# Performance work log

Hardware: AMD Instinct MI355X
Metric: run time of the kernel (lower is better)

## Reference

```python
import jax, jax.numpy as jnp
import numpy as np

N = 50000        # nodes
E = 800000       # edges (avg degree 16)
B = 128          # graphs in batch
NODE_F, EDGE_F, GLOB_F = 16, 8, 32
H = 64           # hidden_dim
L = 4            # num_layers
C = 9            # threshold classes
NG, GE = 20, 16  # num gate types, gate embedding dim
MSG_IN = H + EDGE_F + GE   # 88
UPD_IN = 2 * H             # 128


def _ln(x, g, b):
    mu = x.mean(-1, keepdims=True)
    v = ((x - mu) ** 2).mean(-1, keepdims=True)
    return (x - mu) / jnp.sqrt(v + 1e-5) * g + b


def setup_inputs() -> dict:
    key = jax.random.key(0)
    ks = jax.random.split(key, 24)
    w = lambda k, shp: (jax.random.normal(k, shp, jnp.float32) * 0.05)
    inp = {
        'x': jax.random.normal(ks[0], (N, NODE_F), jnp.float32),
        'edge_index': jax.random.randint(ks[1], (2, E), 0, N, jnp.int32),
        'edge_attr': jax.random.normal(ks[2], (E, EDGE_F), jnp.float32),
        'edge_gate_type': jax.random.randint(ks[3], (E,), 0, NG, jnp.int32),
        'batch': jnp.sort(jax.random.randint(ks[4], (N,), 0, B, jnp.int32)),
        'global_features': jax.random.normal(ks[5], (B, GLOB_F), jnp.float32),
        # node_embed
        'W_embed': w(ks[6], (NODE_F, H)), 'b_embed': jnp.zeros((H,), jnp.float32),
        'g_eln': jnp.ones((H,), jnp.float32), 'b_eln': jnp.zeros((H,), jnp.float32),
        # message-passing layers (stacked over L)
        'mp_gate_emb': w(ks[7], (L, NG, GE)),
        'mp_W_msg': w(ks[8], (L, MSG_IN, H)), 'mp_b_msg': jnp.zeros((L, H), jnp.float32),
        'mp_W_upd': w(ks[9], (L, UPD_IN, H)), 'mp_b_upd': jnp.zeros((L, H), jnp.float32),
        # global_proj
        'W_gproj': w(ks[10], (GLOB_F, H)), 'b_gproj': jnp.zeros((H,), jnp.float32),
        'g_gln': jnp.ones((H,), jnp.float32), 'b_gln': jnp.zeros((H,), jnp.float32),
        # combined_mlp
        'W_c1': w(ks[11], (3 * H + H, 2 * H)), 'b_c1': jnp.zeros((2 * H,), jnp.float32),
        'g_cln': jnp.ones((2 * H,), jnp.float32), 'b_cln': jnp.zeros((2 * H,), jnp.float32),
        'W_c2': w(ks[12], (2 * H, H)), 'b_c2': jnp.zeros((H,), jnp.float32),
        # head
        'W_head': w(ks[13], (H, C)), 'b_head': jnp.zeros((C,), jnp.float32),
    }
    return inp


def reference(x, edge_index, edge_attr, edge_gate_type, batch, global_features,
              W_embed, b_embed, g_eln, b_eln,
              mp_gate_emb, mp_W_msg, mp_b_msg, mp_W_upd, mp_b_upd,
              W_gproj, b_gproj, g_gln, b_gln,
              W_c1, b_c1, g_cln, b_cln, W_c2, b_c2, W_head, b_head):
    n_nodes = x.shape[0]
    n_graphs = global_features.shape[0]
    # node embed (dropout = identity in eval)
    h = _ln(jax.nn.relu(x @ W_embed + b_embed), g_eln, b_eln)  # [N,H]
    src, dst = edge_index[0], edge_index[1]
    for l in range(mp_W_msg.shape[0]):
        ge = mp_gate_emb[l][edge_gate_type]                     # [E,GE] gather
        m_in = jnp.concatenate([h[src], edge_attr, ge], axis=-1)  # [E,MSG_IN]
        m = jax.nn.relu(m_in @ mp_W_msg[l] + mp_b_msg[l])          # [E,H]
        agg = jax.ops.segment_sum(m, dst, num_segments=n_nodes)   # [N,H] scatter-add
        h_new = jnp.concatenate([h, agg], axis=-1) @ mp_W_upd[l] + mp_b_upd[l]
        h = h + h_new                                              # residual
    # multi global pooling
    ones = jnp.ones((n_nodes,), h.dtype)
    counts = jax.ops.segment_sum(ones, batch, num_segments=n_graphs)[:, None]
    h_sum = jax.ops.segment_sum(h, batch, num_segments=n_graphs)
    h_mean = h_sum / jnp.maximum(counts, 1.0)
    h_max = jax.ops.segment_max(h, batch, num_segments=n_graphs)
    h_max = jnp.where(counts > 0, h_max, 0.0)
    h_graph = jnp.concatenate([h_mean, h_max, h_sum], axis=-1)   # [B,3H]
    g = _ln(jax.nn.relu(global_features @ W_gproj + b_gproj), g_gln, b_gln)
    c = jnp.concatenate([h_graph, g], axis=-1)                   # [B,4H]
    c = jax.nn.relu(c @ W_c1 + b_c1)
    c = _ln(c, g_cln, b_cln)
    c = jax.nn.relu(c @ W_c2 + b_c2)
    return c @ W_head + b_head                                   # [B,C]
```

## Files before the change

kernel.cpp:

```cpp
#include <hip/hip_runtime.h>

__device__ __forceinline__ int rfl(int v) { return __builtin_amdgcn_readfirstlane(v); }

__device__ __forceinline__ int lower_bound_dev(const int* __restrict__ a, int n, int v) {
  int lo = 0, hi = n;
  while (lo < hi) { int mid = (lo + hi) >> 1; if (a[mid] < v) lo = mid + 1; else hi = mid; }
  return lo;
}

__global__ void zero_kernel(int4* __restrict__ p, int n4) {
  int i = blockIdx.x * 256 + threadIdx.x;
  if (i < n4) p[i] = make_int4(0, 0, 0, 0);
}

__global__ void count_pack_kernel(const int* __restrict__ dst, const int* __restrict__ src,
                                  const int* __restrict__ gt, int* __restrict__ counts,
                                  int* __restrict__ epack0, int E) {
  int e = blockIdx.x * 256 + threadIdx.x;
  if (e < E) {
    atomicAdd(&counts[dst[e]], 1);
    epack0[e] = (gt[e] << 20) | src[e];
  }
}

__global__ __launch_bounds__(256) void scan_phase1(const int* __restrict__ counts,
                                                   int* __restrict__ row_ptr,
                                                   int* __restrict__ blocksums, int n) {
  int tid = threadIdx.x;
  int i0 = blockIdx.x * 1024 + tid * 4;
  int4 c = make_int4(0, 0, 0, 0);
  if (i0 + 3 < n) {
    c = *(const int4*)(counts + i0);
  } else {
    if (i0 + 0 < n) c.x = counts[i0 + 0];
    if (i0 + 1 < n) c.y = counts[i0 + 1];
    if (i0 + 2 < n) c.z = counts[i0 + 2];
    if (i0 + 3 < n) c.w = counts[i0 + 3];
  }
  int s = c.x + c.y + c.z + c.w;
  int lane = tid & 63, wave = tid >> 6;
  int v = s;
  for (int o = 1; o < 64; o <<= 1) { int u = __shfl_up(v, o); if (lane >= o) v += u; }
  __shared__ int wsum[4];
  if (lane == 63) wsum[wave] = v;
  __syncthreads();
  int woff = 0;
  for (int w = 0; w < wave; w++) woff += wsum[w];
  int excl = woff + (v - s);
  if (tid == 255) blocksums[blockIdx.x] = woff + v;
  int p0 = excl, p1 = p0 + c.x, p2 = p1 + c.y, p3 = p2 + c.z;
  if (i0 + 3 < n) {
    *(int4*)(row_ptr + i0) = make_int4(p0, p1, p2, p3);
  } else {
    if (i0 + 0 < n) row_ptr[i0 + 0] = p0;
    if (i0 + 1 < n) row_ptr[i0 + 1] = p1;
    if (i0 + 2 < n) row_ptr[i0 + 2] = p2;
    if (i0 + 3 < n) row_ptr[i0 + 3] = p3;
  }
}

__global__ __launch_bounds__(64) void scan_phase2(int* __restrict__ blocksums, int nb) {
  int carry = 0;
  for (int base = 0; base < nb; base += 64) {
    int i = base + (int)threadIdx.x;
    int v = (i < nb) ? blocksums[i] : 0;
    int inc = v;
    for (int o = 1; o < 64; o <<= 1) { int u = __shfl_up(inc, o); if ((int)threadIdx.x >= o) inc += u; }
    if (i < nb) blocksums[i] = carry + inc - v;
    carry += __shfl(inc, 63);
  }
}

__global__ __launch_bounds__(256) void scan_phase3(int* __restrict__ row_ptr,
                                                   const int* __restrict__ blocksums,
                                                   int* __restrict__ nextp, int n, int E) {
  int i = blockIdx.x * 256 + threadIdx.x;
  if (i < n) {
    int v = row_ptr[i] + blocksums[i >> 10];
    row_ptr[i] = v;
    nextp[i] = v;
  }
  if (i == 0) row_ptr[n] = E;
}

#define SP_EDGES_PER_BLOCK 2048
__global__ __launch_bounds__(256) void scatter_perm_binned(const int* __restrict__ dst,
                                                           int* __restrict__ nextp,
                                                           int* __restrict__ perm,
                                                           int E, int n_nodes) {
  int phase = blockIdx.x & 7;
  int chunk = blockIdx.x >> 3;
  int lo = (int)(((long long)phase * n_nodes) >> 3);
  int hi = (int)(((long long)(phase + 1) * n_nodes) >> 3);
  int base = chunk * SP_EDGES_PER_BLOCK + threadIdx.x * 8;
#pragma unroll
  for (int half = 0; half < 2; half++) {
    int b = base + half * 4;
    if (b >= E) break;
    int4 d;
    if (b + 3 < E) {
      d = *(const int4*)(dst + b);
    } else {
      d.x = dst[b];
      d.y = (b + 1 < E) ? dst[b + 1] : -1;
      d.z = (b + 2 < E) ? dst[b + 2] : -1;
      d.w = (b + 3 < E) ? dst[b + 3] : -1;
    }
    if (d.x >= lo && d.x < hi) { int p = atomicAdd(&nextp[d.x], 1); perm[p] = b + 0; }
    if (d.y >= lo && d.y < hi) { int p = atomicAdd(&nextp[d.y], 1); perm[p] = b + 1; }
    if (d.z >= lo && d.z < hi) { int p = atomicAdd(&nextp[d.z], 1); perm[p] = b + 2; }
    if (d.w >= lo && d.w < hi) { int p = atomicAdd(&nextp[d.w], 1); perm[p] = b + 3; }
  }
}

__global__ void gather_build(const int* __restrict__ perm, const int* __restrict__ epack0,
                             const float* __restrict__ edge_attr,
                             int* __restrict__ epack, float* __restrict__ eap, int E) {
  int idx = blockIdx.x * 256 + threadIdx.x;
  if (idx < E) {
    int e = perm[idx];
    epack[idx] = epack0[e];
    const float4* s = (const float4*)(edge_attr + (size_t)e * 8);
    float4 a0 = s[0], a1 = s[1];
    float4* d = (float4*)(eap + (size_t)idx * 8);
    d[0] = a0; d[1] = a1;
  }
}

__global__ void gew_kernel(const float* __restrict__ gate_emb, const float* __restrict__ W_msg,
                           float* __restrict__ geW, int nrows) {
  int tid = threadIdx.x;
  int lane = tid & 63;
  int row = blockIdx.x * 4 + (tid >> 6);
  if (row >= nrows) return;
  int l = row / 20, t = row % 20;
  const float* ge = gate_emb + ((size_t)l * 20 + t) * 16;
  const float* W3 = W_msg + (size_t)l * 88 * 64 + 72 * 64;
  float acc = 0.f;
#pragma unroll
  for (int k = 0; k < 16; k++) acc = fmaf(ge[k], W3[(size_t)k * 64 + lane], acc);
  geW[(size_t)row * 64 + lane] = acc;
}

__global__ __launch_bounds__(256) void embed_kernel(const float* __restrict__ x,
                                                    const float* __restrict__ W,
                                                    const float* __restrict__ b,
                                                    const float* __restrict__ gamma,
                                                    const float* __restrict__ beta,
                                                    float* __restrict__ h, int n_nodes) {
  __shared__ float Ws[16 * 64];
  int tid = threadIdx.x;
  for (int i = tid; i < 16 * 64; i += 256) Ws[i] = W[i];
  __syncthreads();
  int lane = tid & 63;
  int n = blockIdx.x * 4 + (tid >> 6);
  if (n >= n_nodes) return;
  const float* xr = x + (size_t)n * 16;
  float acc = b[lane];
#pragma unroll
  for (int k = 0; k < 16; k++) acc = fmaf(xr[k], Ws[k * 64 + lane], acc);
  acc = fmaxf(acc, 0.f);
  float s = acc;
  for (int o = 32; o; o >>= 1) s += __shfl_xor(s, o);
  float mu = s * (1.f / 64.f);
  float d = acc - mu;
  float v = d * d;
  for (int o = 32; o; o >>= 1) v += __shfl_xor(v, o);
  float r = rsqrtf(v * (1.f / 64.f) + 1e-5f);
  h[(size_t)n * 64 + lane] = d * r * gamma[lane] + beta[lane];
}

__global__ __launch_bounds__(256) void nodelin_kernel(const float* __restrict__ A,
                                                      const float* __restrict__ W,
                                                      float* __restrict__ C, int n_nodes) {
  __shared__ float As[64 * 64];
  int tid = threadIdx.x;
  int n0 = blockIdx.x * 64;
#pragma unroll
  for (int i = 0; i < 4; i++) {
    int flat = (tid + i * 256) * 4;
    int r = flat >> 6, k = flat & 63;
    float4 f = make_float4(0.f, 0.f, 0.f, 0.f);
    int n = n0 + r;
    if (n < n_nodes) f = *(const float4*)(A + (size_t)n * 64 + k);
    int rp = r ^ (((k >> 2) & 7) << 2);
    As[(k + 0) * 64 + rp] = f.x;
    As[(k + 1) * 64 + rp] = f.y;
    As[(k + 2) * 64 + rp] = f.z;
    As[(k + 3) * 64 + rp] = f.w;
  }
  __syncthreads();
  int tx = tid & 15, ty = tid >> 4;
  float acc[4][4] = {{0.f}};
  const float4* WV = (const float4*)W;
#pragma unroll 4
  for (int k = 0; k < 64; k++) {
    float4 a = *(const float4*)&As[k * 64 + ((ty * 4) ^ (((k >> 2) & 7) << 2))];
    float4 bb = WV[k * 16 + tx];
    float av[4] = {a.x, a.y, a.z, a.w};
    float bv[4] = {bb.x, bb.y, bb.z, bb.w};
#pragma unroll
    for (int i = 0; i < 4; i++)
#pragma unroll
      for (int j = 0; j < 4; j++) acc[i][j] = fmaf(av[i], bv[j], acc[i][j]);
  }
#pragma unroll
  for (int i = 0; i < 4; i++) {
    int n = n0 + ty * 4 + i;
    if (n < n_nodes) {
      float4 o = make_float4(acc[i][0], acc[i][1], acc[i][2], acc[i][3]);
      *(float4*)&C[(size_t)n * 64 + tx * 4] = o;
    }
  }
}

__global__ __launch_bounds__(256, 4) void edge_kernel(const float* __restrict__ hW,
                                                      const int* __restrict__ epack,
                                                      const float* __restrict__ eap,
                                                      const int* __restrict__ row_ptr,
                                                      const float* __restrict__ W_msg_l,
                                                      const float* __restrict__ b_msg_l,
                                                      const float* __restrict__ geW_l,
                                                      float* __restrict__ agg, int n_nodes) {
  int tid = threadIdx.x;
  int lane = tid & 63;
  int n = blockIdx.x * 4 + (tid >> 6);
  if (n >= n_nodes) return;
  float w2[8];
#pragma unroll
  for (int k = 0; k < 8; k++) w2[k] = W_msg_l[(size_t)(64 + k) * 64 + lane];
  float bm = b_msg_l[lane];
  int beg = rfl(row_ptr[n]);
  int end = rfl(row_ptr[n + 1]);
  float acc0 = 0.f, acc1 = 0.f, acc2 = 0.f, acc3 = 0.f;
  int idx = beg;
  for (; idx + 4 <= end; idx += 4) {
    int p0 = rfl(epack[idx + 0]);
    int p1 = rfl(epack[idx + 1]);
    int p2 = rfl(epack[idx + 2]);
    int p3 = rfl(epack[idx + 3]);
    int s0 = p0 & 0xFFFFF, t0 = p0 >> 20;
    int s1 = p1 & 0xFFFFF, t1 = p1 >> 20;
    int s2 = p2 & 0xFFFFF, t2 = p2 >> 20;
    int s3 = p3 & 0xFFFFF, t3 = p3 >> 20;
    float g0 = hW[(size_t)s0 * 64 + lane];
    float g1 = hW[(size_t)s1 * 64 + lane];
    float g2 = hW[(size_t)s2 * 64 + lane];
    float g3 = hW[(size_t)s3 * 64 + lane];
    float e0 = geW_l[t0 * 64 + lane];
    float e1 = geW_l[t1 * 64 + lane];
    float e2 = geW_l[t2 * 64 + lane];
    float e3 = geW_l[t3 * 64 + lane];
    const float4* ep = (const float4*)(eap + (size_t)idx * 8);
    float4 a00 = ep[0], a01 = ep[1], a10 = ep[2], a11 = ep[3];
    float4 a20 = ep[4], a21 = ep[5], a30 = ep[6], a31 = ep[7];
    float v0 = g0 + e0 + bm;
    v0 = fmaf(a00.x, w2[0], v0); v0 = fmaf(a00.y, w2[1], v0);
    v0 = fmaf(a00.z, w2[2], v0); v0 = fmaf(a00.w, w2[3], v0);
    v0 = fmaf(a01.x, w2[4], v0); v0 = fmaf(a01.y, w2[5], v0);
    v0 = fmaf(a01.z, w2[6], v0); v0 = fmaf(a01.w, w2[7], v0);
    float v1 = g1 + e1 + bm;
    v1 = fmaf(a10.x, w2[0], v1); v1 = fmaf(a10.y, w2[1], v1);
    v1 = fmaf(a10.z, w2[2], v1); v1 = fmaf(a10.w, w2[3], v1);
    v1 = fmaf(a11.x, w2[4], v1); v1 = fmaf(a11.y, w2[5], v1);
    v1 = fmaf(a11.z, w2[6], v1); v1 = fmaf(a11.w, w2[7], v1);
    float v2 = g2 + e2 + bm;
    v2 = fmaf(a20.x, w2[0], v2); v2 = fmaf(a20.y, w2[1], v2);
    v2 = fmaf(a20.z, w2[2], v2); v2 = fmaf(a20.w, w2[3], v2);
    v2 = fmaf(a21.x, w2[4], v2); v2 = fmaf(a21.y, w2[5], v2);
    v2 = fmaf(a21.z, w2[6], v2); v2 = fmaf(a21.w, w2[7], v2);
    float v3 = g3 + e3 + bm;
    v3 = fmaf(a30.x, w2[0], v3); v3 = fmaf(a30.y, w2[1], v3);
    v3 = fmaf(a30.z, w2[2], v3); v3 = fmaf(a30.w, w2[3], v3);
    v3 = fmaf(a31.x, w2[4], v3); v3 = fmaf(a31.y, w2[5], v3);
    v3 = fmaf(a31.z, w2[6], v3); v3 = fmaf(a31.w, w2[7], v3);
    acc0 += fmaxf(v0, 0.f);
    acc1 += fmaxf(v1, 0.f);
    acc2 += fmaxf(v2, 0.f);
    acc3 += fmaxf(v3, 0.f);
  }
  for (; idx < end; idx++) {
    int p = rfl(epack[idx]);
    int s = p & 0xFFFFF, t = p >> 20;
    const float4* ep = (const float4*)(eap + (size_t)idx * 8);
    float4 a0 = ep[0], a1 = ep[1];
    float g = hW[(size_t)s * 64 + lane];
    float v = g + geW_l[t * 64 + lane] + bm;
    v = fmaf(a0.x, w2[0], v); v = fmaf(a0.y, w2[1], v);
    v = fmaf(a0.z, w2[2], v); v = fmaf(a0.w, w2[3], v);
    v = fmaf(a1.x, w2[4], v); v = fmaf(a1.y, w2[5], v);
    v = fmaf(a1.z, w2[6], v); v = fmaf(a1.w, w2[7], v);
    acc0 += fmaxf(v, 0.f);
  }
  agg[(size_t)n * 64 + lane] = (acc0 + acc1) + (acc2 + acc3);
}

__global__ __launch_bounds__(256) void update_fused_kernel(const float* __restrict__ h,
                                                           const float* __restrict__ agg,
                                                           const float* __restrict__ Wu,
                                                           const float* __restrict__ bu,
                                                           const float* __restrict__ W1next,
                                                           float* __restrict__ h_out,
                                                           float* __restrict__ hW_out,
                                                           int n_nodes) {
  __shared__ float As[128 * 64];
  int tid = threadIdx.x;
  int n0 = blockIdx.x * 64;
#pragma unroll
  for (int i = 0; i < 8; i++) {
    int flat = (tid + i * 256) * 4;
    int r = flat >> 7, k = flat & 127;
    float4 f = make_float4(0.f, 0.f, 0.f, 0.f);
    int n = n0 + r;
    if (n < n_nodes) {
      const float* sp = (k < 64) ? (h + (size_t)n * 64 + k) : (agg + (size_t)n * 64 + (k - 64));
      f = *(const float4*)sp;
    }
    int rp = r ^ (((k >> 2) & 7) << 2);
    As[(k + 0) * 64 + rp] = f.x;
    As[(k + 1) * 64 + rp] = f.y;
    As[(k + 2) * 64 + rp] = f.z;
    As[(k + 3) * 64 + rp] = f.w;
  }
  __syncthreads();
  int tx = tid & 15, ty = tid >> 4;
  float acc[4][4] = {{0.f}};
  const float4* WuV = (const float4*)Wu;
#pragma unroll 4
  for (int k = 0; k < 128; k++) {
    float4 a = *(const float4*)&As[k * 64 + ((ty * 4) ^ (((k >> 2) & 7) << 2))];
    float4 bb = WuV[k * 16 + tx];
    float av[4] = {a.x, a.y, a.z, a.w};
    float bv[4] = {bb.x, bb.y, bb.z, bb.w};
#pragma unroll
    for (int i = 0; i < 4; i++)
#pragma unroll
      for (int j = 0; j < 4; j++) acc[i][j] = fmaf(av[i], bv[j], acc[i][j]);
  }
  float hnew[4][4];
  float4 bv4 = *(const float4*)&bu[tx * 4];
#pragma unroll
  for (int i = 0; i < 4; i++) {
    int n = n0 + ty * 4 + i;
    if (n < n_nodes) {
      float4 hv = *(const float4*)&h[(size_t)n * 64 + tx * 4];
      hnew[i][0] = hv.x + acc[i][0] + bv4.x;
      hnew[i][1] = hv.y + acc[i][1] + bv4.y;
      hnew[i][2] = hv.z + acc[i][2] + bv4.z;
      hnew[i][3] = hv.w + acc[i][3] + bv4.w;
      float4 o = make_float4(hnew[i][0], hnew[i][1], hnew[i][2], hnew[i][3]);
      *(float4*)&h_out[(size_t)n * 64 + tx * 4] = o;
    } else {
      hnew[i][0] = hnew[i][1] = hnew[i][2] = hnew[i][3] = 0.f;
    }
  }
  if (W1next) {
    __syncthreads();
#pragma unroll
    for (int i = 0; i < 4; i++) {
      float4 o = make_float4(hnew[i][0], hnew[i][1], hnew[i][2], hnew[i][3]);
      *(float4*)&As[(ty * 4 + i) * 68 + tx * 4] = o;
    }
    __syncthreads();
    float acc2[4][4] = {{0.f}};
    const float4* W1V = (const float4*)W1next;
#pragma unroll 4
    for (int k = 0; k < 64; k++) {
      float av[4];
#pragma unroll
      for (int i = 0; i < 4; i++) av[i] = As[(ty * 4 + i) * 68 + k];
      float4 bb = W1V[k * 16 + tx];
      float bv[4] = {bb.x, bb.y, bb.z, bb.w};
#pragma unroll
      for (int i = 0; i < 4; i++)
#pragma unroll
        for (int j = 0; j < 4; j++) acc2[i][j] = fmaf(av[i], bv[j], acc2[i][j]);
    }
#pragma unroll
    for (int i = 0; i < 4; i++) {
      int n = n0 + ty * 4 + i;
      if (n < n_nodes) {
        float4 o = make_float4(acc2[i][0], acc2[i][1], acc2[i][2], acc2[i][3]);
        *(float4*)&hW_out[(size_t)n * 64 + tx * 4] = o;
      }
    }
  }
}

#define PSPLIT 8
__global__ __launch_bounds__(256) void pool_partial(const float* __restrict__ h,
                                                    const int* __restrict__ batch,
                                                    float* __restrict__ partials, int n_nodes) {
  int b = blockIdx.x / PSPLIT;
  int p = blockIdx.x % PSPLIT;
  int tid = threadIdx.x;
  int lane = tid & 63, wave = tid >> 6;
  __shared__ int se[2];
  if (tid < 2) se[tid] = lower_bound_dev(batch, n_nodes, b + tid);
  __syncthreads();
  int start = se[0], len = se[1] - se[0];
  int c0 = start + (int)(((long long)p * len) / PSPLIT);
  int c1 = start + (int)(((long long)(p + 1) * len) / PSPLIT);
  float s = 0.f, m = -INFINITY;
  for (int i = c0 + wave; i < c1; i += 4) {
    float v = h[(size_t)i * 64 + lane];
    s += v;
    m = fmaxf(m, v);
  }
  __shared__ float ss[4][64], mm[4][64];
  ss[wave][lane] = s;
  mm[wave][lane] = m;
  __syncthreads();
  if (wave == 0) {
    float sum = ss[0][lane] + ss[1][lane] + ss[2][lane] + ss[3][lane];
    float mx = fmaxf(fmaxf(mm[0][lane], mm[1][lane]), fmaxf(mm[2][lane], mm[3][lane]));
    float* dst = partials + ((size_t)(b * PSPLIT + p) * 2) * 64;
    dst[lane] = sum;
    dst[64 + lane] = mx;
  }
}

__global__ __launch_bounds__(256) void pool_mlp_final(
    const float* __restrict__ partials, const int* __restrict__ batch,
    const float* __restrict__ glob,
    const float* __restrict__ W_gproj, const float* __restrict__ b_gproj,
    const float* __restrict__ g_gln, const float* __restrict__ b_gln,
    const float* __restrict__ W_c1, const float* __restrict__ b_c1,
    const float* __restrict__ g_cln, const float* __restrict__ b_cln,
    const float* __restrict__ W_c2, const float* __restrict__ b_c2,
    const float* __restrict__ W_head, const float* __restrict__ b_head,
    float* __restrict__ out, int n_nodes) {
  int b = blockIdx.x;
  int tid = threadIdx.x;
  int lane = tid & 63, wave = tid >> 6;
  __shared__ int se[2];
  if (tid < 2) se[tid] = lower_bound_dev(batch, n_nodes, b + tid);
  __shared__ float c[256];
  __shared__ float c1s[128];
  __shared__ float c2s[64];
  __shared__ float sred[2][2];
  __syncthreads();
  int cnt = se[1] - se[0];
  if (wave == 0) {
    const float* pp = partials + ((size_t)b * PSPLIT * 2) * 64;
    float sum = 0.f, mx = -INFINITY;
#pragma unroll
    for (int p = 0; p < PSPLIT; p++) {
      sum += pp[(size_t)p * 128 + lane];
      mx = fmaxf(mx, pp[(size_t)p * 128 + 64 + lane]);
    }
    float mean = (cnt > 0) ? sum / (float)cnt : 0.f;
    if (cnt == 0) { mx = 0.f; sum = 0.f; }
    c[lane] = mean;
    c[64 + lane] = mx;
    c[128 + lane] = sum;
  } else if (wave == 1) {
    const float* gf = glob + (size_t)b * 32;
    float acc = b_gproj[lane];
#pragma unroll
    for (int k = 0; k < 32; k++) acc = fmaf(gf[k], W_gproj[(size_t)k * 64 + lane], acc);
    acc = fmaxf(acc, 0.f);
    float sg = acc;
    for (int o = 32; o; o >>= 1) sg += __shfl_xor(sg, o);
    float mu = sg * (1.f / 64.f);
    float d = acc - mu;
    float vv = d * d;
    for (int o = 32; o; o >>= 1) vv += __shfl_xor(vv, o);
    float r = rsqrtf(vv * (1.f / 64.f) + 1e-5f);
    c[192 + lane] = d * r * g_gln[lane] + b_gln[lane];
  }
  __syncthreads();
  float acc1v = 0.f;
  if (tid < 128) {
    acc1v = b_c1[tid];
    for (int k = 0; k < 256; k++) acc1v = fmaf(c[k], W_c1[(size_t)k * 128 + tid], acc1v);
    acc1v = fmaxf(acc1v, 0.f);
    float srd = acc1v;
    for (int o = 32; o; o >>= 1) srd += __shfl_xor(srd, o);
    if (lane == 0) sred[0][wave] = srd;
  }
  __syncthreads();
  float mu = (sred[0][0] + sred[0][1]) * (1.f / 128.f);
  float d1 = 0.f;
  if (tid < 128) {
    d1 = acc1v - mu;
    float vv = d1 * d1;
    for (int o = 32; o; o >>= 1) vv += __shfl_xor(vv, o);
    if (lane == 0) sred[1][wave] = vv;
  }
  __syncthreads();
  float var = (sred[1][0] + sred[1][1]) * (1.f / 128.f);
  if (tid < 128) c1s[tid] = d1 * rsqrtf(var + 1e-5f) * g_cln[tid] + b_cln[tid];
  __syncthreads();
  if (tid < 64) {
    float a2 = b_c2[tid];
    for (int k = 0; k < 128; k++) a2 = fmaf(c1s[k], W_c2[(size_t)k * 64 + tid], a2);
    c2s[tid] = fmaxf(a2, 0.f);
  }
  __syncthreads();
  if (tid < 9) {
    float a3 = b_head[tid];
#pragma unroll
    for (int k = 0; k < 64; k++) a3 = fmaf(c2s[k], W_head[(size_t)k * 9 + tid], a3);
    out[(size_t)b * 9 + tid] = a3;
  }
}

extern "C" void kernel_launch(void* const* d_in, const int* in_sizes, int n_in,
                              void* d_out, int out_size, void* d_ws, size_t ws_size,
                              hipStream_t stream) {
  const float* x       = (const float*)d_in[0];
  const int* edge_index= (const int*)d_in[1];
  const float* edge_attr=(const float*)d_in[2];
  const int* gtype     = (const int*)d_in[3];
  const int* batch     = (const int*)d_in[4];
  const float* glob    = (const float*)d_in[5];
  const float* W_embed = (const float*)d_in[6];
  const float* b_embed = (const float*)d_in[7];
  const float* g_eln   = (const float*)d_in[8];
  const float* b_eln   = (const float*)d_in[9];
  const float* gate_emb= (const float*)d_in[10];
  const float* W_msg   = (const float*)d_in[11];
  const float* b_msg   = (const float*)d_in[12];
  const float* W_upd   = (const float*)d_in[13];
  const float* b_upd   = (const float*)d_in[14];
  const float* W_gproj = (const float*)d_in[15];
  const float* b_gproj = (const float*)d_in[16];
  const float* g_gln   = (const float*)d_in[17];
  const float* b_gln   = (const float*)d_in[18];
  const float* W_c1    = (const float*)d_in[19];
  const float* b_c1    = (const float*)d_in[20];
  const float* g_cln   = (const float*)d_in[21];
  const float* b_cln   = (const float*)d_in[22];
  const float* W_c2    = (const float*)d_in[23];
  const float* b_c2    = (const float*)d_in[24];
  const float* W_head  = (const float*)d_in[25];
  const float* b_head  = (const float*)d_in[26];

  const int N = in_sizes[0] / 16;
  const int E = in_sizes[1] / 2;
  const int B = in_sizes[5] / 32;
  const int L = in_sizes[12] / 64;

  const int* src = edge_index;
  const int* dst = edge_index + E;

  char* ws = (char*)d_ws;
  size_t off = 0;
  auto alloc = [&](size_t bytes) -> void* {
    void* p = ws + off;
    off += (bytes + 255) & ~(size_t)255;
    return p;
  };
  float* h      = (float*)alloc((size_t)N * 64 * 4);
  float* hW     = (float*)alloc((size_t)N * 64 * 4);
  float* agg    = (float*)alloc((size_t)N * 64 * 4);
  float* geW    = (float*)alloc((size_t)L * 20 * 64 * 4);
  float* partials = (float*)alloc((size_t)B * PSPLIT * 2 * 64 * 4);
  int nC4 = (N + 3) / 4;
  int* counts   = (int*)alloc((size_t)nC4 * 16);
  int* row_ptr  = (int*)alloc((size_t)(N + 1) * 4);
  int* nextp    = (int*)alloc((size_t)N * 4);
  int nb = (N + 1023) / 1024;
  int* blocksums= (int*)alloc((size_t)nb * 4);
  int* perm     = (int*)alloc((size_t)E * 4);
  int* epack0   = (int*)alloc((size_t)E * 4);
  int* epack    = (int*)alloc((size_t)E * 4);
  float* eap    = (float*)alloc((size_t)E * 8 * 4);

  zero_kernel<<<(nC4 + 255) / 256, 256, 0, stream>>>((int4*)counts, nC4);
  count_pack_kernel<<<(E + 255) / 256, 256, 0, stream>>>(dst, src, gtype, counts, epack0, E);
  scan_phase1<<<nb, 256, 0, stream>>>(counts, row_ptr, blocksums, N);
  scan_phase2<<<1, 64, 0, stream>>>(blocksums, nb);
  scan_phase3<<<(N + 255) / 256, 256, 0, stream>>>(row_ptr, blocksums, nextp, N, E);
  {
    int nchunks = (E + SP_EDGES_PER_BLOCK - 1) / SP_EDGES_PER_BLOCK;
    scatter_perm_binned<<<nchunks * 8, 256, 0, stream>>>(dst, nextp, perm, E, N);
  }
  gather_build<<<(E + 255) / 256, 256, 0, stream>>>(perm, epack0, edge_attr, epack, eap, E);
  gew_kernel<<<(L * 20 + 3) / 4, 256, 0, stream>>>(gate_emb, W_msg, geW, L * 20);
  embed_kernel<<<(N + 3) / 4, 256, 0, stream>>>(x, W_embed, b_embed, g_eln, b_eln, h, N);

  nodelin_kernel<<<(N + 63) / 64, 256, 0, stream>>>(h, W_msg, hW, N);
  for (int l = 0; l < L; l++) {
    edge_kernel<<<(N + 3) / 4, 256, 0, stream>>>(hW, epack, eap, row_ptr,
                                                 W_msg + (size_t)l * 88 * 64, b_msg + (size_t)l * 64,
                                                 geW + (size_t)l * 20 * 64, agg, N);
    const float* W1next = (l + 1 < L) ? (W_msg + (size_t)(l + 1) * 88 * 64) : nullptr;
    update_fused_kernel<<<(N + 63) / 64, 256, 0, stream>>>(h, agg, W_upd + (size_t)l * 128 * 64,
                                                           b_upd + (size_t)l * 64, W1next, h, hW, N);
  }

  pool_partial<<<B * PSPLIT, 256, 0, stream>>>(h, batch, partials, N);
  pool_mlp_final<<<B, 256, 0, stream>>>(partials, batch, glob, W_gproj, b_gproj, g_gln, b_gln,
                                        W_c1, b_c1, g_cln, b_cln, W_c2, b_c2,
                                        W_head, b_head, (float*)d_out, N);
}
```

Measured before the change: 445.6 us.

## Pre-bucket edges by destination range before scatter into CSR permutation

Replaces the eight-pass binned scatter, where every block rereads all dst indices and filters by node range, with a bucketing kernel that writes (edge, dst) pairs into eight range buckets using shared-memory counters and one global atomic per bucket per block. A second kernel then scatters each bucket's entries into perm with atomics on nextp, so each edge is processed once while locality by node range is kept. It adds a bucket buffer and an extra launch. Buckets have a fixed capacity, so edges beyond it would be silently dropped for skewed dst distributions.

Result: slower. 487.2 us (+9.3%).

```diff
diff --git a/kernel.cpp b/kernel.cpp
--- a/kernel.cpp
+++ b/kernel.cpp
@@ -83,34 +83,52 @@
   if (i == 0) row_ptr[n] = E;
 }
 
-#define SP_EDGES_PER_BLOCK 2048
-__global__ __launch_bounds__(256) void scatter_perm_binned(const int* __restrict__ dst,
-                                                           int* __restrict__ nextp,
-                                                           int* __restrict__ perm,
-                                                           int E, int n_nodes) {
-  int phase = blockIdx.x & 7;
+__global__ __launch_bounds__(256) void bucket_kernel(const int* __restrict__ dst,
+                                                     int* __restrict__ bcount,
+                                                     int2* __restrict__ buckets,
+                                                     int E, int n_nodes, int capb) {
+  __shared__ int lcount[8];
+  __shared__ int lbase[8];
+  int tid = threadIdx.x;
+  if (tid < 8) lcount[tid] = 0;
+  __syncthreads();
+  int e = blockIdx.x * 256 + tid;
+  int b = 0, d = 0, slot = 0;
+  bool ok = (e < E);
+  if (ok) {
+    d = dst[e];
+    b = (int)(((long long)d * 8) / n_nodes);
+    slot = atomicAdd(&lcount[b], 1);
+  }
+  __syncthreads();
+  if (tid < 8) lbase[tid] = atomicAdd(&bcount[tid], lcount[tid]);
+  __syncthreads();
+  if (ok) {
+    int pos = lbase[b] + slot;
+    if (pos < capb) buckets[(size_t)b * capb + pos] = make_int2(e, d);
+  }
+}
+
+__global__ __launch_bounds__(256) void scatter_from_buckets(const int2* __restrict__ buckets,
+                                                            const int* __restrict__ bcount,
+                                                            int* __restrict__ nextp,
+                                                            int* __restrict__ perm,
+                                                            int capb) {
+  int b = blockIdx.x & 7;
   int chunk = blockIdx.x >> 3;
-  int lo = (int)(((long long)phase * n_nodes) >> 3);
-  int hi = (int)(((long long)(phase + 1) * n_nodes) >> 3);
-  int base = chunk * SP_EDGES_PER_BLOCK + threadIdx.x * 8;
-#pragma unroll
-  for (int half = 0; half < 2; half++) {
-    int b = base + half * 4;
-    if (b >= E) break;
-    int4 d;
-    if (b + 3 < E) {
-      d = *(const int4*)(dst + b);
-    } else {
-      d.x = dst[b];
-      d.y = (b + 1 < E) ? dst[b + 1] : -1;
-      d.z = (b + 2 < E) ? dst[b + 2] : -1;
-      d.w = (b + 3 < E) ? dst[b + 3] : -1;
-    }
-    if (d.x >= lo && d.x < hi) { int p = atomicAdd(&nextp[d.x], 1); perm[p] = b + 0; }
-    if (d.y >= lo && d.y < hi) { int p = atomicAdd(&nextp[d.y], 1); perm[p] = b + 1; }
-    if (d.z >= lo && d.z < hi) { int p = atomicAdd(&nextp[d.z], 1); perm[p] = b + 2; }
-    if (d.w >= lo && d.w < hi) { int p = atomicAdd(&nextp[d.w], 1); perm[p] = b + 3; }
-  }
+  int cnt = bcount[b];
+  if (cnt > capb) cnt = capb;
+  int i0 = chunk * 1024 + threadIdx.x * 4;
+  if (i0 >= cnt) return;
+  const int4* bp = (const int4*)(buckets + (size_t)b * capb);
+  int4 q0 = bp[i0 >> 1];
+  int4 q1 = bp[(i0 >> 1) + 1];
+  {
+    int p = atomicAdd(&nextp[q0.y], 1); perm[p] = q0.x;
+  }
+  if (i0 + 1 < cnt) { int p = atomicAdd(&nextp[q0.w], 1); perm[p] = q0.z; }
+  if (i0 + 2 < cnt) { int p = atomicAdd(&nextp[q1.y], 1); perm[p] = q1.x; }
+  if (i0 + 3 < cnt) { int p = atomicAdd(&nextp[q1.w], 1); perm[p] = q1.z; }
 }
 
 __global__ void gather_build(const int* __restrict__ perm, const int* __restrict__ epack0,
@@ -558,7 +576,8 @@
   float* geW    = (float*)alloc((size_t)L * 20 * 64 * 4);
   float* partials = (float*)alloc((size_t)B * PSPLIT * 2 * 64 * 4);
   int nC4 = (N + 3) / 4;
-  int* counts   = (int*)alloc((size_t)nC4 * 16);
+  int* counts   = (int*)alloc((size_t)nC4 * 16 + 32);
+  int* bcount   = counts + nC4 * 4;
   int* row_ptr  = (int*)alloc((size_t)(N + 1) * 4);
   int* nextp    = (int*)alloc((size_t)N * 4);
   int nb = (N + 1023) / 1024;
@@ -567,15 +586,19 @@
   int* epack0   = (int*)alloc((size_t)E * 4);
   int* epack    = (int*)alloc((size_t)E * 4);
   float* eap    = (float*)alloc((size_t)E * 8 * 4);
-
-  zero_kernel<<<(nC4 + 255) / 256, 256, 0, stream>>>((int4*)counts, nC4);
+  int capb = E / 8 + E / 32 + 64;
+  int2* buckets = (int2*)alloc((size_t)capb * 8 * 8);
+
+  int nZ4 = nC4 + 2;
+  zero_kernel<<<(nZ4 + 255) / 256, 256, 0, stream>>>((int4*)counts, nZ4);
   count_pack_kernel<<<(E + 255) / 256, 256, 0, stream>>>(dst, src, gtype, counts, epack0, E);
   scan_phase1<<<nb, 256, 0, stream>>>(counts, row_ptr, blocksums, N);
   scan_phase2<<<1, 64, 0, stream>>>(blocksums, nb);
   scan_phase3<<<(N + 255) / 256, 256, 0, stream>>>(row_ptr, blocksums, nextp, N, E);
+  bucket_kernel<<<(E + 255) / 256, 256, 0, stream>>>(dst, bcount, buckets, E, N, capb);
   {
-    int nchunks = (E + SP_EDGES_PER_BLOCK - 1) / SP_EDGES_PER_BLOCK;
-    scatter_perm_binned<<<nchunks * 8, 256, 0, stream>>>(dst, nextp, perm, E, N);
+    int chunksB = (capb + 1023) / 1024;
+    scatter_from_buckets<<<chunksB * 8, 256, 0, stream>>>(buckets, bcount, nextp, perm, capb);
   }
   gather_build<<<(E + 255) / 256, 256, 0, stream>>>(perm, epack0, edge_attr, epack, eap, E);
   gew_kernel<<<(L * 20 + 3) / 4, 256, 0, stream>>>(gate_emb, W_msg, geW, L * 20);
```
